# Optimization experiments

Measured on AMD Instinct MI355X. Metric: run time of the kernel, lower is better.

The kernel has to match this reference:

```python
import jax, jax.numpy as jnp
import numpy as np

N_NODES = 100000
D_IN = 64
D_OUT = 64
N_EDGES = 1000000
NEG_SLOPE = 0.2  # PyG GATConv default negative_slope


def _glorot(key, shape):
    fan_in, fan_out = shape[0], shape[-1]
    lim = jnp.sqrt(6.0 / (fan_in + fan_out)).astype(jnp.float32)
    return jax.random.uniform(key, shape, jnp.float32, -lim, lim)


def gat_layer(x, edges, W, a_src, a_dst):
    """Single-head GATConv (bias=False, add_self_loops=True), eval mode."""
    n = x.shape[0]
    h = x @ W  # [N, D]
    loops = jnp.arange(n, dtype=edges.dtype)
    src = jnp.concatenate([edges[0], loops])  # self-loops appended
    dst = jnp.concatenate([edges[1], loops])
    # per-edge attention logits
    e = jnp.take(h @ a_src, src) + jnp.take(h @ a_dst, dst)  # [E+N]
    e = jax.nn.leaky_relu(e, NEG_SLOPE)
    # softmax over incoming edges of each destination node
    m = jax.ops.segment_max(e, dst, num_segments=n)
    w = jnp.exp(e - m[dst])
    denom = jax.ops.segment_sum(w, dst, num_segments=n)
    alpha = w / denom[dst]
    # weighted scatter-aggregate of source features
    return jax.ops.segment_sum(alpha[:, None] * h[src], dst, num_segments=n)


def setup_inputs() -> dict:
    key = jax.random.key(0)
    k = jax.random.split(key, 8)
    x = jax.random.normal(k[0], (N_NODES, D_IN), jnp.float32)
    edges = jax.random.randint(k[1], (2, N_EDGES), 0, N_NODES, dtype=jnp.int64)
    W1 = _glorot(k[2], (D_IN, D_IN))
    as1 = _glorot(k[3], (D_IN,))
    ad1 = _glorot(k[4], (D_IN,))
    W2 = _glorot(k[5], (D_IN, D_OUT))
    as2 = _glorot(k[6], (D_OUT,))
    ad2 = _glorot(k[7], (D_OUT,))
    return {"x": x, "edges": edges, "W1": W1, "as1": as1, "ad1": ad1,
            "W2": W2, "as2": as2, "ad2": ad2}


def reference(x, edges, W1, as1, ad1, W2, as2, ad2):
    h = gat_layer(x, edges, W1, as1, ad1)
    # F.dropout(p=0.2) is identity in eval mode
    return gat_layer(h, edges, W2, as2, ad2)
```

## Files before the change

### kernel.cpp

```cpp
#include <hip/hip_runtime.h>

#define NEG_SLOPE 0.2f

typedef unsigned int uint32;

__device__ __forceinline__ uint32 pack2bf(float a, float b) {
    uint32 ua = __float_as_uint(a);
    uint32 ub = __float_as_uint(b);
    ua += 0x7fffu + ((ua >> 16) & 1u);
    ub += 0x7fffu + ((ub >> 16) & 1u);
    return (ua >> 16) | (ub & 0xffff0000u);
}


__global__ void count_pos_kernel(const int* __restrict__ dst, int* __restrict__ deg,
                                 int* __restrict__ pos, int E) {
    int i = blockIdx.x * blockDim.x + threadIdx.x;
    if (i < E) pos[i] = atomicAdd(&deg[dst[i]], 1);
}

__global__ void scanA_kernel(const int* __restrict__ deg, int* __restrict__ binc,
                             int* __restrict__ bsum, int n) {
    __shared__ int ws[4];
    int tid = threadIdx.x;
    int i = blockIdx.x * 256 + tid;
    int lane = tid & 63, wid = tid >> 6;
    int x = (i < n) ? (deg[i] + 1) : 0;
    #pragma unroll
    for (int d = 1; d < 64; d <<= 1) { int t = __shfl_up(x, d); if (lane >= d) x += t; }
    if (lane == 63) ws[wid] = x;
    __syncthreads();
    int wofs = 0;
    for (int w = 0; w < wid; ++w) wofs += ws[w];
    x += wofs;
    if (i < n) binc[i] = x;
    if (tid == 255) bsum[blockIdx.x] = x;
}

__global__ void scanB_kernel(int* __restrict__ bsum, int nb) {
    __shared__ int ws[8];
    __shared__ int run_s;
    int tid = threadIdx.x;
    int lane = tid & 63, wid = tid >> 6;
    if (tid == 0) run_s = 0;
    __syncthreads();
    for (int base = 0; base < nb; base += 512) {
        int i = base + tid;
        int v = (i < nb) ? bsum[i] : 0;
        int x = v;
        #pragma unroll
        for (int d = 1; d < 64; d <<= 1) { int t = __shfl_up(x, d); if (lane >= d) x += t; }
        if (lane == 63) ws[wid] = x;
        __syncthreads();
        int wofs = 0;
        for (int w = 0; w < wid; ++w) wofs += ws[w];
        x += wofs;
        int run = run_s;
        if (i < nb) bsum[i] = x + run;
        __syncthreads();
        if (tid == 511) run_s = run + x;
        __syncthreads();
    }
}

__global__ void scanC_kernel(const int* __restrict__ binc, const int* __restrict__ bsumS,
                             int* __restrict__ off, int n) {
    int i = blockIdx.x * 256 + threadIdx.x;
    if (i < n) off[i + 1] = binc[i] + (blockIdx.x ? bsumS[blockIdx.x - 1] : 0);
    if (i == 0) off[0] = 0;
}


__global__ __launch_bounds__(256) void gemm_fill_kernel(
        const float* __restrict__ X, const float* __restrict__ W,
        const float* __restrict__ a_src, const float* __restrict__ a_dst,
        uint32* __restrict__ Hb, float* __restrict__ S, float* __restrict__ D, int n,
        const int* __restrict__ src, const int* __restrict__ dst,
        const int* __restrict__ pos, const int* __restrict__ off,
        int* __restrict__ csr, int E, int nblkG) {
    __shared__ float Xs[64][65];
    __shared__ float Wl[64 * 64];

    if (blockIdx.x >= nblkG) {
        int i = (blockIdx.x - nblkG) * 256 + threadIdx.x;
        int total = E + n;
        if (i >= total) return;
        if (i < E) {
            csr[off[dst[i]] + pos[i]] = src[i];
        } else {
            int v = i - E;
            csr[off[v + 1] - 1] = v;
        }
        return;
    }

    int tid = threadIdx.x;
    int row0 = blockIdx.x * 64;
    {
        const float4* W4 = reinterpret_cast<const float4*>(W);
        float4* Wl4 = reinterpret_cast<float4*>(Wl);
        for (int i = tid; i < 1024; i += 256) Wl4[i] = W4[i];
    }
    {
        for (int i = tid; i < 1024; i += 256) {
            int r = i >> 4;
            int c4 = (i & 15) * 4;
            int row = row0 + r;
            float4 xv = {0.f, 0.f, 0.f, 0.f};
            if (row < n) xv = *reinterpret_cast<const float4*>(&X[(size_t)row * 64 + c4]);
            Xs[r][c4 + 0] = xv.x; Xs[r][c4 + 1] = xv.y;
            Xs[r][c4 + 2] = xv.z; Xs[r][c4 + 3] = xv.w;
        }
    }
    __syncthreads();

    int c4 = (tid & 15) * 4;
    int r4 = (tid >> 4) * 4;
    float acc[4][4] = {};
    #pragma unroll 4
    for (int k = 0; k < 64; ++k) {
        float4 wv = *reinterpret_cast<const float4*>(&Wl[k * 64 + c4]);
        float x0 = Xs[r4 + 0][k];
        float x1 = Xs[r4 + 1][k];
        float x2 = Xs[r4 + 2][k];
        float x3 = Xs[r4 + 3][k];
        acc[0][0] = fmaf(x0, wv.x, acc[0][0]); acc[0][1] = fmaf(x0, wv.y, acc[0][1]);
        acc[0][2] = fmaf(x0, wv.z, acc[0][2]); acc[0][3] = fmaf(x0, wv.w, acc[0][3]);
        acc[1][0] = fmaf(x1, wv.x, acc[1][0]); acc[1][1] = fmaf(x1, wv.y, acc[1][1]);
        acc[1][2] = fmaf(x1, wv.z, acc[1][2]); acc[1][3] = fmaf(x1, wv.w, acc[1][3]);
        acc[2][0] = fmaf(x2, wv.x, acc[2][0]); acc[2][1] = fmaf(x2, wv.y, acc[2][1]);
        acc[2][2] = fmaf(x2, wv.z, acc[2][2]); acc[2][3] = fmaf(x2, wv.w, acc[2][3]);
        acc[3][0] = fmaf(x3, wv.x, acc[3][0]); acc[3][1] = fmaf(x3, wv.y, acc[3][1]);
        acc[3][2] = fmaf(x3, wv.z, acc[3][2]); acc[3][3] = fmaf(x3, wv.w, acc[3][3]);
    }
    #pragma unroll
    for (int i = 0; i < 4; ++i) {
        int row = row0 + r4 + i;
        if (row < n) {
            uint2 p;
            p.x = pack2bf(acc[i][0], acc[i][1]);
            p.y = pack2bf(acc[i][2], acc[i][3]);
            *reinterpret_cast<uint2*>(&Hb[(size_t)row * 32 + (c4 >> 1)]) = p;
        }
    }
    float4 av = *reinterpret_cast<const float4*>(&a_src[c4]);
    float4 bv = *reinterpret_cast<const float4*>(&a_dst[c4]);
    #pragma unroll
    for (int i = 0; i < 4; ++i) {
        float ps = acc[i][0] * av.x + acc[i][1] * av.y + acc[i][2] * av.z + acc[i][3] * av.w;
        float pd = acc[i][0] * bv.x + acc[i][1] * bv.y + acc[i][2] * bv.z + acc[i][3] * bv.w;
        #pragma unroll
        for (int o = 1; o < 16; o <<= 1) {
            ps += __shfl_xor(ps, o);
            pd += __shfl_xor(pd, o);
        }
        int row = row0 + r4 + i;
        if ((tid & 15) == 0 && row < n) { S[row] = ps; D[row] = pd; }
    }
}


__global__ __launch_bounds__(256) void gemm_sd_kernel(
        const float* __restrict__ X, const float* __restrict__ W,
        const float* __restrict__ a_src, const float* __restrict__ a_dst,
        uint32* __restrict__ Hb, float* __restrict__ S, float* __restrict__ D, int n) {
    __shared__ float Xs[64][65];
    __shared__ float Wl[64 * 64];
    int tid = threadIdx.x;
    int row0 = blockIdx.x * 64;
    {
        const float4* W4 = reinterpret_cast<const float4*>(W);
        float4* Wl4 = reinterpret_cast<float4*>(Wl);
        for (int i = tid; i < 1024; i += 256) Wl4[i] = W4[i];
    }
    {
        for (int i = tid; i < 1024; i += 256) {
            int r = i >> 4;
            int c4 = (i & 15) * 4;
            int row = row0 + r;
            float4 xv = {0.f, 0.f, 0.f, 0.f};
            if (row < n) xv = *reinterpret_cast<const float4*>(&X[(size_t)row * 64 + c4]);
            Xs[r][c4 + 0] = xv.x; Xs[r][c4 + 1] = xv.y;
            Xs[r][c4 + 2] = xv.z; Xs[r][c4 + 3] = xv.w;
        }
    }
    __syncthreads();
    int c4 = (tid & 15) * 4;
    int r4 = (tid >> 4) * 4;
    float acc[4][4] = {};
    #pragma unroll 4
    for (int k = 0; k < 64; ++k) {
        float4 wv = *reinterpret_cast<const float4*>(&Wl[k * 64 + c4]);
        float x0 = Xs[r4 + 0][k];
        float x1 = Xs[r4 + 1][k];
        float x2 = Xs[r4 + 2][k];
        float x3 = Xs[r4 + 3][k];
        acc[0][0] = fmaf(x0, wv.x, acc[0][0]); acc[0][1] = fmaf(x0, wv.y, acc[0][1]);
        acc[0][2] = fmaf(x0, wv.z, acc[0][2]); acc[0][3] = fmaf(x0, wv.w, acc[0][3]);
        acc[1][0] = fmaf(x1, wv.x, acc[1][0]); acc[1][1] = fmaf(x1, wv.y, acc[1][1]);
        acc[1][2] = fmaf(x1, wv.z, acc[1][2]); acc[1][3] = fmaf(x1, wv.w, acc[1][3]);
        acc[2][0] = fmaf(x2, wv.x, acc[2][0]); acc[2][1] = fmaf(x2, wv.y, acc[2][1]);
        acc[2][2] = fmaf(x2, wv.z, acc[2][2]); acc[2][3] = fmaf(x2, wv.w, acc[2][3]);
        acc[3][0] = fmaf(x3, wv.x, acc[3][0]); acc[3][1] = fmaf(x3, wv.y, acc[3][1]);
        acc[3][2] = fmaf(x3, wv.z, acc[3][2]); acc[3][3] = fmaf(x3, wv.w, acc[3][3]);
    }
    #pragma unroll
    for (int i = 0; i < 4; ++i) {
        int row = row0 + r4 + i;
        if (row < n) {
            uint2 p;
            p.x = pack2bf(acc[i][0], acc[i][1]);
            p.y = pack2bf(acc[i][2], acc[i][3]);
            *reinterpret_cast<uint2*>(&Hb[(size_t)row * 32 + (c4 >> 1)]) = p;
        }
    }
    float4 av = *reinterpret_cast<const float4*>(&a_src[c4]);
    float4 bv = *reinterpret_cast<const float4*>(&a_dst[c4]);
    #pragma unroll
    for (int i = 0; i < 4; ++i) {
        float ps = acc[i][0] * av.x + acc[i][1] * av.y + acc[i][2] * av.z + acc[i][3] * av.w;
        float pd = acc[i][0] * bv.x + acc[i][1] * bv.y + acc[i][2] * bv.z + acc[i][3] * bv.w;
        #pragma unroll
        for (int o = 1; o < 16; o <<= 1) {
            ps += __shfl_xor(ps, o);
            pd += __shfl_xor(pd, o);
        }
        int row = row0 + r4 + i;
        if ((tid & 15) == 0 && row < n) { S[row] = ps; D[row] = pd; }
    }
}


__global__ __launch_bounds__(256) void aggregate_kernel(
        const uint32* __restrict__ Hb, const float* __restrict__ S,
        const float* __restrict__ D,
        const int* __restrict__ off, const int* __restrict__ csr,
        float* __restrict__ out, int n) {
    int v = blockIdx.x * 4 + (threadIdx.x >> 6);
    int lane = threadIdx.x & 63;
    if (v >= n) return;
    int beg = off[v], end = off[v + 1];
    int deg = end - beg;
    float dv = D[v];
    int t = lane & 7, g = lane >> 3;
    float acc[8] = {};

    if (deg <= 64) {
        int sreg = 0;
        float e = -INFINITY;
        if (lane < deg) {
            sreg = csr[beg + lane];
            e = S[sreg] + dv;
            e = (e > 0.f) ? e : NEG_SLOPE * e;
        }
        float m = e;
        #pragma unroll
        for (int o = 32; o > 0; o >>= 1) m = fmaxf(m, __shfl_xor(m, o));
        float w = (lane < deg) ? __expf(e - m) : 0.f;
        float dsum = w;
        #pragma unroll
        for (int o = 32; o > 0; o >>= 1) dsum += __shfl_xor(dsum, o);
        w *= (1.f / dsum);
        for (int base = 0; base < deg; base += 8) {
            int jj = base + g;
            int jidx = (jj < deg) ? jj : 0;
            float a = __shfl(w, jidx);
            int s = __shfl(sreg, jidx);
            if (jj < deg) {
                uint4 u = *reinterpret_cast<const uint4*>(&Hb[(size_t)s * 32 + t * 4]);
                acc[0] = fmaf(a, __uint_as_float(u.x << 16), acc[0]);
                acc[1] = fmaf(a, __uint_as_float(u.x & 0xffff0000u), acc[1]);
                acc[2] = fmaf(a, __uint_as_float(u.y << 16), acc[2]);
                acc[3] = fmaf(a, __uint_as_float(u.y & 0xffff0000u), acc[3]);
                acc[4] = fmaf(a, __uint_as_float(u.z << 16), acc[4]);
                acc[5] = fmaf(a, __uint_as_float(u.z & 0xffff0000u), acc[5]);
                acc[6] = fmaf(a, __uint_as_float(u.w << 16), acc[6]);
                acc[7] = fmaf(a, __uint_as_float(u.w & 0xffff0000u), acc[7]);
            }
        }
    } else {
        float m = -INFINITY;
        for (int j = beg + lane; j < end; j += 64) {
            float e = S[csr[j]] + dv;
            e = (e > 0.f) ? e : NEG_SLOPE * e;
            m = fmaxf(m, e);
        }
        #pragma unroll
        for (int o = 32; o > 0; o >>= 1) m = fmaxf(m, __shfl_xor(m, o));
        float dsum = 0.f;
        for (int j = beg + lane; j < end; j += 64) {
            float e = S[csr[j]] + dv;
            e = (e > 0.f) ? e : NEG_SLOPE * e;
            dsum += __expf(e - m);
        }
        #pragma unroll
        for (int o = 32; o > 0; o >>= 1) dsum += __shfl_xor(dsum, o);
        float inv = 1.f / dsum;
        for (int base = 0; base < deg; base += 8) {
            int jj = base + g;
            if (jj < deg) {
                int s = csr[beg + jj];
                float e = S[s] + dv;
                e = (e > 0.f) ? e : NEG_SLOPE * e;
                float a = __expf(e - m) * inv;
                uint4 u = *reinterpret_cast<const uint4*>(&Hb[(size_t)s * 32 + t * 4]);
                acc[0] = fmaf(a, __uint_as_float(u.x << 16), acc[0]);
                acc[1] = fmaf(a, __uint_as_float(u.x & 0xffff0000u), acc[1]);
                acc[2] = fmaf(a, __uint_as_float(u.y << 16), acc[2]);
                acc[3] = fmaf(a, __uint_as_float(u.y & 0xffff0000u), acc[3]);
                acc[4] = fmaf(a, __uint_as_float(u.z << 16), acc[4]);
                acc[5] = fmaf(a, __uint_as_float(u.z & 0xffff0000u), acc[5]);
                acc[6] = fmaf(a, __uint_as_float(u.w << 16), acc[6]);
                acc[7] = fmaf(a, __uint_as_float(u.w & 0xffff0000u), acc[7]);
            }
        }
    }
    #pragma unroll
    for (int o = 8; o <= 32; o <<= 1) {
        #pragma unroll
        for (int k = 0; k < 8; ++k) acc[k] += __shfl_xor(acc[k], o);
    }
    if (g == 0) {
        float4 o0 = { acc[0], acc[1], acc[2], acc[3] };
        float4 o1 = { acc[4], acc[5], acc[6], acc[7] };
        *reinterpret_cast<float4*>(&out[(size_t)v * 64 + t * 8 + 0]) = o0;
        *reinterpret_cast<float4*>(&out[(size_t)v * 64 + t * 8 + 4]) = o1;
    }
}


extern "C" void kernel_launch(void* const* d_in, const int* in_sizes, int n_in,
                              void* d_out, int out_size, void* d_ws, size_t ws_size,
                              hipStream_t stream) {
    const float* x   = (const float*)d_in[0];
    const int*   e   = (const int*)d_in[1];
    const float* W1  = (const float*)d_in[2];
    const float* as1 = (const float*)d_in[3];
    const float* ad1 = (const float*)d_in[4];
    const float* W2  = (const float*)d_in[5];
    const float* as2 = (const float*)d_in[6];
    const float* ad2 = (const float*)d_in[7];
    float* out = (float*)d_out;

    const int N = in_sizes[0] / 64;
    const int E = in_sizes[1] / 2;
    const int* src = e;
    const int* dst = e + E;

    uint32* Hb  = (uint32*)d_ws;
    float* S    = (float*)(Hb + (size_t)N * 32);
    float* D    = S + N;
    int* deg    = (int*)(D + N);
    int* off    = deg + N;
    int* pos    = off + N + 1;
    int* csr    = pos + E;
    int* binc   = csr + (size_t)E + N;
    int* bsum   = binc + N;
    float* z1   = out;

    const int B = 256;
    int nblkN = (N + B - 1) / B;
    int nblkE = (E + B - 1) / B;
    int nblkT = (E + N + B - 1) / B;
    int nblkG = (N + 63) / 64;
    int nblkW = (N + 3) / 4;

    hipMemsetAsync(deg, 0, (size_t)N * sizeof(int), stream);
    count_pos_kernel<<<nblkE, B, 0, stream>>>(dst, deg, pos, E);
    scanA_kernel<<<nblkN, B, 0, stream>>>(deg, binc, bsum, N);
    scanB_kernel<<<1, 512, 0, stream>>>(bsum, nblkN);
    scanC_kernel<<<nblkN, B, 0, stream>>>(binc, bsum, off, N);

    gemm_fill_kernel<<<nblkG + nblkT, B, 0, stream>>>(
        x, W1, as1, ad1, Hb, S, D, N, src, dst, pos, off, csr, E, nblkG);

    aggregate_kernel<<<nblkW, B, 0, stream>>>(Hb, S, D, off, csr, z1, N);
    gemm_sd_kernel<<<nblkG, B, 0, stream>>>(z1, W2, as2, ad2, Hb, S, D, N);
    aggregate_kernel<<<nblkW, B, 0, stream>>>(Hb, S, D, off, csr, out, N);
}
```

Baseline: 204.3 us.

## Process two nodes per wavefront in aggregation and refactor shared GEMM body

The aggregation kernel now assigns one 32-lane half-wavefront per destination node, so each wavefront handles two nodes, with a fallback loop for nodes whose degree exceeds 32. The GEMM is factored into a shared device function that uses float4 shared-memory reads with a 68-float padded row. The memset is replaced by an init kernel, z1 moves into the workspace, and bounds clamps are added on csr indices. The aim is better lane utilization for low-degree nodes (average degree about 11); the cost is extra shuffles, clamping work, and a divergent fallback path.

```diff
diff --git a/kernel.cpp b/kernel.cpp
--- a/kernel.cpp
+++ b/kernel.cpp
@@ -12,6 +12,11 @@
     return (ua >> 16) | (ub & 0xffff0000u);
 }
 
+
+__global__ void init_deg_kernel(int* __restrict__ deg, int n) {
+    int i = blockIdx.x * blockDim.x + threadIdx.x;
+    if (i < n) deg[i] = 0;
+}
 
 __global__ void count_pos_kernel(const int* __restrict__ dst, int* __restrict__ deg,
                                  int* __restrict__ pos, int E) {
@@ -71,31 +76,13 @@
 }
 
 
-__global__ __launch_bounds__(256) void gemm_fill_kernel(
+__device__ __forceinline__ void gemm_body(
         const float* __restrict__ X, const float* __restrict__ W,
         const float* __restrict__ a_src, const float* __restrict__ a_dst,
-        uint32* __restrict__ Hb, float* __restrict__ S, float* __restrict__ D, int n,
-        const int* __restrict__ src, const int* __restrict__ dst,
-        const int* __restrict__ pos, const int* __restrict__ off,
-        int* __restrict__ csr, int E, int nblkG) {
-    __shared__ float Xs[64][65];
-    __shared__ float Wl[64 * 64];
-
-    if (blockIdx.x >= nblkG) {
-        int i = (blockIdx.x - nblkG) * 256 + threadIdx.x;
-        int total = E + n;
-        if (i >= total) return;
-        if (i < E) {
-            csr[off[dst[i]] + pos[i]] = src[i];
-        } else {
-            int v = i - E;
-            csr[off[v + 1] - 1] = v;
-        }
-        return;
-    }
-
+        uint32* __restrict__ Hb, float* __restrict__ S, float* __restrict__ D,
+        int n, int tile, float (*Xs)[68], float* Wl) {
     int tid = threadIdx.x;
-    int row0 = blockIdx.x * 64;
+    int row0 = tile * 64;
     {
         const float4* W4 = reinterpret_cast<const float4*>(W);
         float4* Wl4 = reinterpret_cast<float4*>(Wl);
@@ -108,8 +95,7 @@
             int row = row0 + r;
             float4 xv = {0.f, 0.f, 0.f, 0.f};
             if (row < n) xv = *reinterpret_cast<const float4*>(&X[(size_t)row * 64 + c4]);
-            Xs[r][c4 + 0] = xv.x; Xs[r][c4 + 1] = xv.y;
-            Xs[r][c4 + 2] = xv.z; Xs[r][c4 + 3] = xv.w;
+            *reinterpret_cast<float4*>(&Xs[r][c4]) = xv;
         }
     }
     __syncthreads();
@@ -118,20 +104,23 @@
     int r4 = (tid >> 4) * 4;
     float acc[4][4] = {};
     #pragma unroll 4
-    for (int k = 0; k < 64; ++k) {
-        float4 wv = *reinterpret_cast<const float4*>(&Wl[k * 64 + c4]);
-        float x0 = Xs[r4 + 0][k];
-        float x1 = Xs[r4 + 1][k];
-        float x2 = Xs[r4 + 2][k];
-        float x3 = Xs[r4 + 3][k];
-        acc[0][0] = fmaf(x0, wv.x, acc[0][0]); acc[0][1] = fmaf(x0, wv.y, acc[0][1]);
-        acc[0][2] = fmaf(x0, wv.z, acc[0][2]); acc[0][3] = fmaf(x0, wv.w, acc[0][3]);
-        acc[1][0] = fmaf(x1, wv.x, acc[1][0]); acc[1][1] = fmaf(x1, wv.y, acc[1][1]);
-        acc[1][2] = fmaf(x1, wv.z, acc[1][2]); acc[1][3] = fmaf(x1, wv.w, acc[1][3]);
-        acc[2][0] = fmaf(x2, wv.x, acc[2][0]); acc[2][1] = fmaf(x2, wv.y, acc[2][1]);
-        acc[2][2] = fmaf(x2, wv.z, acc[2][2]); acc[2][3] = fmaf(x2, wv.w, acc[2][3]);
-        acc[3][0] = fmaf(x3, wv.x, acc[3][0]); acc[3][1] = fmaf(x3, wv.y, acc[3][1]);
-        acc[3][2] = fmaf(x3, wv.z, acc[3][2]); acc[3][3] = fmaf(x3, wv.w, acc[3][3]);
+    for (int k0 = 0; k0 < 64; k0 += 4) {
+        float x4[4][4];
+        #pragma unroll
+        for (int i = 0; i < 4; ++i)
+            *reinterpret_cast<float4*>(x4[i]) =
+                *reinterpret_cast<const float4*>(&Xs[r4 + i][k0]);
+        #pragma unroll
+        for (int j = 0; j < 4; ++j) {
+            float4 wv = *reinterpret_cast<const float4*>(&Wl[(k0 + j) * 64 + c4]);
+            #pragma unroll
+            for (int i = 0; i < 4; ++i) {
+                acc[i][0] = fmaf(x4[i][j], wv.x, acc[i][0]);
+                acc[i][1] = fmaf(x4[i][j], wv.y, acc[i][1]);
+                acc[i][2] = fmaf(x4[i][j], wv.z, acc[i][2]);
+                acc[i][3] = fmaf(x4[i][j], wv.w, acc[i][3]);
+            }
+        }
     }
     #pragma unroll
     for (int i = 0; i < 4; ++i) {
@@ -160,74 +149,41 @@
 }
 
 
+__global__ __launch_bounds__(256) void gemm_fill_kernel(
+        const float* __restrict__ X, const float* __restrict__ W,
+        const float* __restrict__ a_src, const float* __restrict__ a_dst,
+        uint32* __restrict__ Hb, float* __restrict__ S, float* __restrict__ D, int n,
+        const int* __restrict__ src, const int* __restrict__ dst,
+        const int* __restrict__ pos, const int* __restrict__ off,
+        int* __restrict__ csr, int E, int nblkG) {
+    __shared__ float Xs[64][68];
+    __shared__ float Wl[64 * 64];
+
+    if (blockIdx.x >= nblkG) {
+        int i = (blockIdx.x - nblkG) * 256 + threadIdx.x;
+        int total = E + n;
+        if (i >= total) return;
+        if (i < E) {
+            int idx = off[dst[i]] + pos[i];
+            if ((unsigned)idx < (unsigned)total) csr[idx] = src[i];
+        } else {
+            int v = i - E;
+            int idx = off[v + 1] - 1;
+            if ((unsigned)idx < (unsigned)total) csr[idx] = v;
+        }
+        return;
+    }
+    gemm_body(X, W, a_src, a_dst, Hb, S, D, n, blockIdx.x, Xs, Wl);
+}
+
+
 __global__ __launch_bounds__(256) void gemm_sd_kernel(
         const float* __restrict__ X, const float* __restrict__ W,
         const float* __restrict__ a_src, const float* __restrict__ a_dst,
         uint32* __restrict__ Hb, float* __restrict__ S, float* __restrict__ D, int n) {
-    __shared__ float Xs[64][65];
+    __shared__ float Xs[64][68];
     __shared__ float Wl[64 * 64];
-    int tid = threadIdx.x;
-    int row0 = blockIdx.x * 64;
-    {
-        const float4* W4 = reinterpret_cast<const float4*>(W);
-        float4* Wl4 = reinterpret_cast<float4*>(Wl);
-        for (int i = tid; i < 1024; i += 256) Wl4[i] = W4[i];
-    }
-    {
-        for (int i = tid; i < 1024; i += 256) {
-            int r = i >> 4;
-            int c4 = (i & 15) * 4;
-            int row = row0 + r;
-            float4 xv = {0.f, 0.f, 0.f, 0.f};
-            if (row < n) xv = *reinterpret_cast<const float4*>(&X[(size_t)row * 64 + c4]);
-            Xs[r][c4 + 0] = xv.x; Xs[r][c4 + 1] = xv.y;
-            Xs[r][c4 + 2] = xv.z; Xs[r][c4 + 3] = xv.w;
-        }
-    }
-    __syncthreads();
-    int c4 = (tid & 15) * 4;
-    int r4 = (tid >> 4) * 4;
-    float acc[4][4] = {};
-    #pragma unroll 4
-    for (int k = 0; k < 64; ++k) {
-        float4 wv = *reinterpret_cast<const float4*>(&Wl[k * 64 + c4]);
-        float x0 = Xs[r4 + 0][k];
-        float x1 = Xs[r4 + 1][k];
-        float x2 = Xs[r4 + 2][k];
-        float x3 = Xs[r4 + 3][k];
-        acc[0][0] = fmaf(x0, wv.x, acc[0][0]); acc[0][1] = fmaf(x0, wv.y, acc[0][1]);
-        acc[0][2] = fmaf(x0, wv.z, acc[0][2]); acc[0][3] = fmaf(x0, wv.w, acc[0][3]);
-        acc[1][0] = fmaf(x1, wv.x, acc[1][0]); acc[1][1] = fmaf(x1, wv.y, acc[1][1]);
-        acc[1][2] = fmaf(x1, wv.z, acc[1][2]); acc[1][3] = fmaf(x1, wv.w, acc[1][3]);
-        acc[2][0] = fmaf(x2, wv.x, acc[2][0]); acc[2][1] = fmaf(x2, wv.y, acc[2][1]);
-        acc[2][2] = fmaf(x2, wv.z, acc[2][2]); acc[2][3] = fmaf(x2, wv.w, acc[2][3]);
-        acc[3][0] = fmaf(x3, wv.x, acc[3][0]); acc[3][1] = fmaf(x3, wv.y, acc[3][1]);
-        acc[3][2] = fmaf(x3, wv.z, acc[3][2]); acc[3][3] = fmaf(x3, wv.w, acc[3][3]);
-    }
-    #pragma unroll
-    for (int i = 0; i < 4; ++i) {
-        int row = row0 + r4 + i;
-        if (row < n) {
-            uint2 p;
-            p.x = pack2bf(acc[i][0], acc[i][1]);
-            p.y = pack2bf(acc[i][2], acc[i][3]);
-            *reinterpret_cast<uint2*>(&Hb[(size_t)row * 32 + (c4 >> 1)]) = p;
-        }
-    }
-    float4 av = *reinterpret_cast<const float4*>(&a_src[c4]);
-    float4 bv = *reinterpret_cast<const float4*>(&a_dst[c4]);
-    #pragma unroll
-    for (int i = 0; i < 4; ++i) {
-        float ps = acc[i][0] * av.x + acc[i][1] * av.y + acc[i][2] * av.z + acc[i][3] * av.w;
-        float pd = acc[i][0] * bv.x + acc[i][1] * bv.y + acc[i][2] * bv.z + acc[i][3] * bv.w;
-        #pragma unroll
-        for (int o = 1; o < 16; o <<= 1) {
-            ps += __shfl_xor(ps, o);
-            pd += __shfl_xor(pd, o);
-        }
-        int row = row0 + r4 + i;
-        if ((tid & 15) == 0 && row < n) { S[row] = ps; D[row] = pd; }
-    }
+    gemm_body(X, W, a_src, a_dst, Hb, S, D, n, blockIdx.x, Xs, Wl);
 }
 
 
@@ -236,95 +192,125 @@
         const float* __restrict__ D,
         const int* __restrict__ off, const int* __restrict__ csr,
         float* __restrict__ out, int n) {
-    int v = blockIdx.x * 4 + (threadIdx.x >> 6);
-    int lane = threadIdx.x & 63;
-    if (v >= n) return;
-    int beg = off[v], end = off[v + 1];
-    int deg = end - beg;
-    float dv = D[v];
-    int t = lane & 7, g = lane >> 3;
-    float acc[8] = {};
-
-    if (deg <= 64) {
+    int tid = threadIdx.x;
+    int lane = tid & 63;
+    int sl = lane & 31;
+    int seg = lane >> 5;
+    int wv_ = tid >> 6;
+    int v = blockIdx.x * 8 + wv_ * 2 + seg;
+    bool valid = v < n;
+    int beg = 0, deg = 0;
+    float dv = 0.f;
+    if (valid) { beg = off[v]; deg = off[v + 1] - beg; dv = D[v]; }
+
+    if (__all(deg <= 32)) {
         int sreg = 0;
         float e = -INFINITY;
-        if (lane < deg) {
-            sreg = csr[beg + lane];
-            e = S[sreg] + dv;
-            e = (e > 0.f) ? e : NEG_SLOPE * e;
+        if (sl < deg) {
+            int s0 = csr[beg + sl];
+            sreg = ((unsigned)s0 < (unsigned)n) ? s0 : 0;
+            float t = S[sreg] + dv;
+            e = (t > 0.f) ? t : NEG_SLOPE * t;
         }
         float m = e;
         #pragma unroll
-        for (int o = 32; o > 0; o >>= 1) m = fmaxf(m, __shfl_xor(m, o));
-        float w = (lane < deg) ? __expf(e - m) : 0.f;
+        for (int o = 16; o > 0; o >>= 1) m = fmaxf(m, __shfl_xor(m, o));
+        float w = (sl < deg) ? __expf(e - m) : 0.f;
         float dsum = w;
         #pragma unroll
-        for (int o = 32; o > 0; o >>= 1) dsum += __shfl_xor(dsum, o);
+        for (int o = 16; o > 0; o >>= 1) dsum += __shfl_xor(dsum, o);
         w *= (1.f / dsum);
-        for (int base = 0; base < deg; base += 8) {
-            int jj = base + g;
-            int jidx = (jj < deg) ? jj : 0;
-            float a = __shfl(w, jidx);
-            int s = __shfl(sreg, jidx);
-            if (jj < deg) {
-                uint4 u = *reinterpret_cast<const uint4*>(&Hb[(size_t)s * 32 + t * 4]);
-                acc[0] = fmaf(a, __uint_as_float(u.x << 16), acc[0]);
-                acc[1] = fmaf(a, __uint_as_float(u.x & 0xffff0000u), acc[1]);
-                acc[2] = fmaf(a, __uint_as_float(u.y << 16), acc[2]);
-                acc[3] = fmaf(a, __uint_as_float(u.y & 0xffff0000u), acc[3]);
-                acc[4] = fmaf(a, __uint_as_float(u.z << 16), acc[4]);
-                acc[5] = fmaf(a, __uint_as_float(u.z & 0xffff0000u), acc[5]);
-                acc[6] = fmaf(a, __uint_as_float(u.w << 16), acc[6]);
-                acc[7] = fmaf(a, __uint_as_float(u.w & 0xffff0000u), acc[7]);
-            }
+
+        int t8 = sl & 7, g = sl >> 3;
+        int segbase = seg << 5;
+        float acc[8] = {};
+        int dmax = max(deg, __shfl_xor(deg, 32));
+        int nit = (dmax + 3) >> 2;
+        for (int it = 0; it < nit; ++it) {
+            int jj = (it << 2) + g;
+            int jidx = (jj < deg) ? jj : ((deg > 0) ? (deg - 1) : 0);
+            float a = __shfl(w, segbase + jidx);
+            int s = __shfl(sreg, segbase + jidx);
+            a = (jj < deg) ? a : 0.f;
+            uint4 u = *reinterpret_cast<const uint4*>(&Hb[((size_t)s << 5) + (t8 << 2)]);
+            acc[0] = fmaf(a, __uint_as_float(u.x << 16), acc[0]);
+            acc[1] = fmaf(a, __uint_as_float(u.x & 0xffff0000u), acc[1]);
+            acc[2] = fmaf(a, __uint_as_float(u.y << 16), acc[2]);
+            acc[3] = fmaf(a, __uint_as_float(u.y & 0xffff0000u), acc[3]);
+            acc[4] = fmaf(a, __uint_as_float(u.z << 16), acc[4]);
+            acc[5] = fmaf(a, __uint_as_float(u.z & 0xffff0000u), acc[5]);
+            acc[6] = fmaf(a, __uint_as_float(u.w << 16), acc[6]);
+            acc[7] = fmaf(a, __uint_as_float(u.w & 0xffff0000u), acc[7]);
+        }
+        #pragma unroll
+        for (int o = 8; o <= 16; o <<= 1) {
+            #pragma unroll
+            for (int k = 0; k < 8; ++k) acc[k] += __shfl_xor(acc[k], o);
+        }
+        if (valid && g == 0) {
+            float4 o0 = { acc[0], acc[1], acc[2], acc[3] };
+            float4 o1 = { acc[4], acc[5], acc[6], acc[7] };
+            *reinterpret_cast<float4*>(&out[(size_t)v * 64 + (t8 << 3)]) = o0;
+            *reinterpret_cast<float4*>(&out[(size_t)v * 64 + (t8 << 3) + 4]) = o1;
         }
     } else {
-        float m = -INFINITY;
-        for (int j = beg + lane; j < end; j += 64) {
-            float e = S[csr[j]] + dv;
-            e = (e > 0.f) ? e : NEG_SLOPE * e;
-            m = fmaxf(m, e);
-        }
-        #pragma unroll
-        for (int o = 32; o > 0; o >>= 1) m = fmaxf(m, __shfl_xor(m, o));
-        float dsum = 0.f;
-        for (int j = beg + lane; j < end; j += 64) {
-            float e = S[csr[j]] + dv;
-            e = (e > 0.f) ? e : NEG_SLOPE * e;
-            dsum += __expf(e - m);
-        }
-        #pragma unroll
-        for (int o = 32; o > 0; o >>= 1) dsum += __shfl_xor(dsum, o);
-        float inv = 1.f / dsum;
-        for (int base = 0; base < deg; base += 8) {
-            int jj = base + g;
-            if (jj < deg) {
-                int s = csr[beg + jj];
-                float e = S[s] + dv;
-                e = (e > 0.f) ? e : NEG_SLOPE * e;
-                float a = __expf(e - m) * inv;
-                uint4 u = *reinterpret_cast<const uint4*>(&Hb[(size_t)s * 32 + t * 4]);
-                acc[0] = fmaf(a, __uint_as_float(u.x << 16), acc[0]);
-                acc[1] = fmaf(a, __uint_as_float(u.x & 0xffff0000u), acc[1]);
-                acc[2] = fmaf(a, __uint_as_float(u.y << 16), acc[2]);
-                acc[3] = fmaf(a, __uint_as_float(u.y & 0xffff0000u), acc[3]);
-                acc[4] = fmaf(a, __uint_as_float(u.z << 16), acc[4]);
-                acc[5] = fmaf(a, __uint_as_float(u.z & 0xffff0000u), acc[5]);
-                acc[6] = fmaf(a, __uint_as_float(u.w << 16), acc[6]);
-                acc[7] = fmaf(a, __uint_as_float(u.w & 0xffff0000u), acc[7]);
-            }
-        }
-    }
-    #pragma unroll
-    for (int o = 8; o <= 32; o <<= 1) {
-        #pragma unroll
-        for (int k = 0; k < 8; ++k) acc[k] += __shfl_xor(acc[k], o);
-    }
-    if (g == 0) {
-        float4 o0 = { acc[0], acc[1], acc[2], acc[3] };
-        float4 o1 = { acc[4], acc[5], acc[6], acc[7] };
-        *reinterpret_cast<float4*>(&out[(size_t)v * 64 + t * 8 + 0]) = o0;
-        *reinterpret_cast<float4*>(&out[(size_t)v * 64 + t * 8 + 4]) = o1;
+        for (int it = 0; it < 2; ++it) {
+            int vv = blockIdx.x * 8 + wv_ * 2 + it;
+            if (vv >= n) continue;
+            int beg2 = off[vv], end2 = off[vv + 1];
+            int deg2 = end2 - beg2;
+            float dv2 = D[vv];
+            float m = -INFINITY;
+            for (int j = beg2 + lane; j < end2; j += 64) {
+                int s0 = csr[j]; s0 = ((unsigned)s0 < (unsigned)n) ? s0 : 0;
+                float t = S[s0] + dv2;
+                t = (t > 0.f) ? t : NEG_SLOPE * t;
+                m = fmaxf(m, t);
+            }
+            #pragma unroll
+            for (int o = 32; o > 0; o >>= 1) m = fmaxf(m, __shfl_xor(m, o));
+            float dsum = 0.f;
+            for (int j = beg2 + lane; j < end2; j += 64) {
+                int s0 = csr[j]; s0 = ((unsigned)s0 < (unsigned)n) ? s0 : 0;
+                float t = S[s0] + dv2;
+                t = (t > 0.f) ? t : NEG_SLOPE * t;
+                dsum += __expf(t - m);
+            }
+            #pragma unroll
+            for (int o = 32; o > 0; o >>= 1) dsum += __shfl_xor(dsum, o);
+            float inv = 1.f / dsum;
+            int t8 = lane & 7, g8 = lane >> 3;
+            float acc[8] = {};
+            for (int b = 0; b < deg2; b += 8) {
+                int jj = b + g8;
+                if (jj < deg2) {
+                    int s = csr[beg2 + jj]; s = ((unsigned)s < (unsigned)n) ? s : 0;
+                    float t = S[s] + dv2;
+                    t = (t > 0.f) ? t : NEG_SLOPE * t;
+                    float a = __expf(t - m) * inv;
+                    uint4 u = *reinterpret_cast<const uint4*>(&Hb[((size_t)s << 5) + (t8 << 2)]);
+                    acc[0] = fmaf(a, __uint_as_float(u.x << 16), acc[0]);
+                    acc[1] = fmaf(a, __uint_as_float(u.x & 0xffff0000u), acc[1]);
+                    acc[2] = fmaf(a, __uint_as_float(u.y << 16), acc[2]);
+                    acc[3] = fmaf(a, __uint_as_float(u.y & 0xffff0000u), acc[3]);
+                    acc[4] = fmaf(a, __uint_as_float(u.z << 16), acc[4]);
+                    acc[5] = fmaf(a, __uint_as_float(u.z & 0xffff0000u), acc[5]);
+                    acc[6] = fmaf(a, __uint_as_float(u.w << 16), acc[6]);
+                    acc[7] = fmaf(a, __uint_as_float(u.w & 0xffff0000u), acc[7]);
+                }
+            }
+            #pragma unroll
+            for (int o = 8; o <= 32; o <<= 1) {
+                #pragma unroll
+                for (int k = 0; k < 8; ++k) acc[k] += __shfl_xor(acc[k], o);
+            }
+            if (g8 == 0) {
+                float4 o0 = { acc[0], acc[1], acc[2], acc[3] };
+                float4 o1 = { acc[4], acc[5], acc[6], acc[7] };
+                *reinterpret_cast<float4*>(&out[(size_t)vv * 64 + (t8 << 3)]) = o0;
+                *reinterpret_cast<float4*>(&out[(size_t)vv * 64 + (t8 << 3) + 4]) = o1;
+            }
+        }
     }
 }
 
@@ -348,7 +334,8 @@
     const int* dst = e + E;
 
     uint32* Hb  = (uint32*)d_ws;
-    float* S    = (float*)(Hb + (size_t)N * 32);
+    float* z1   = (float*)(Hb + (size_t)N * 32);
+    float* S    = z1 + (size_t)N * 64;
     float* D    = S + N;
     int* deg    = (int*)(D + N);
     int* off    = deg + N;
@@ -356,16 +343,15 @@
     int* csr    = pos + E;
     int* binc   = csr + (size_t)E + N;
     int* bsum   = binc + N;
-    float* z1   = out;
 
     const int B = 256;
     int nblkN = (N + B - 1) / B;
     int nblkE = (E + B - 1) / B;
     int nblkT = (E + N + B - 1) / B;
     int nblkG = (N + 63) / 64;
-    int nblkW = (N + 3) / 4;
-
-    hipMemsetAsync(deg, 0, (size_t)N * sizeof(int), stream);
+    int nblkA = (N + 7) / 8;
+
+    init_deg_kernel<<<nblkN, B, 0, stream>>>(deg, N);
     count_pos_kernel<<<nblkE, B, 0, stream>>>(dst, deg, pos, E);
     scanA_kernel<<<nblkN, B, 0, stream>>>(deg, binc, bsum, N);
     scanB_kernel<<<1, 512, 0, stream>>>(bsum, nblkN);
@@ -374,7 +360,7 @@
     gemm_fill_kernel<<<nblkG + nblkT, B, 0, stream>>>(
         x, W1, as1, ad1, Hb, S, D, N, src, dst, pos, off, csr, E, nblkG);
 
-    aggregate_kernel<<<nblkW, B, 0, stream>>>(Hb, S, D, off, csr, z1, N);
+    aggregate_kernel<<<nblkA, B, 0, stream>>>(Hb, S, D, off, csr, z1, N);
     gemm_sd_kernel<<<nblkG, B, 0, stream>>>(z1, W2, as2, ad2, Hb, S, D, N);
-    aggregate_kernel<<<nblkW, B, 0, stream>>>(Hb, S, D, off, csr, out, N);
-}
+    aggregate_kernel<<<nblkA, B, 0, stream>>>(Hb, S, D, off, csr, out, N);
+}
```

Result: faster. 172.1 us (-15.7%).
